# Kernel tuning notes

Hardware: AMD Instinct MI355X
Metric: run time of the kernel (lower is better)

Reference implementation:

```python
import jax, jax.numpy as jnp
import numpy as np

N_NODES = 100_000
D_FEAT = 512
N_EDGES = 3_200_000
L1, L2 = 32, 16
EPS = 1e-7


def setup_inputs() -> dict:
    key = jax.random.key(0)
    k = jax.random.split(key, 6)
    X = jax.random.normal(k[0], (N_NODES, D_FEAT), jnp.float32)
    # Xavier-uniform-ish init, as in get_weight_initial
    b1 = np.sqrt(6.0 / (D_FEAT + L1)).astype(np.float32)
    b2 = np.sqrt(6.0 / (L1 + L2)).astype(np.float32)
    W1 = jax.random.uniform(k[1], (D_FEAT, L1), jnp.float32, -b1, b1)
    W2 = jax.random.uniform(k[2], (L1, L2), jnp.float32, -b2, b2)
    lap_rows = jax.random.randint(k[3], (N_EDGES,), 0, N_NODES, jnp.int32)
    lap_cols = jax.random.randint(k[4], (N_EDGES,), 0, N_NODES, jnp.int32)
    # normalized-Laplacian values are small positives
    lap_vals = jax.random.uniform(k[5], (N_EDGES,), jnp.float32) * 0.1
    return {"X": X, "W1": W1, "W2": W2, "lap_rows": lap_rows,
            "lap_cols": lap_cols, "lap_vals": lap_vals}


def reference(X, W1, W2, lap_rows, lap_cols, lap_vals):
    n = X.shape[0]

    def spmm(H):  # Laplacian.mm(H): out[r] += val * H[c]
        return jax.ops.segment_sum(lap_vals[:, None] * H[lap_cols],
                                   lap_rows, num_segments=n)

    # layer 1: SpMM(X @ W1) -> relu
    H = jax.nn.relu(spmm(X @ W1))          # [N, 32]
    # layer 2: SpMM(H @ W2), final act is identity
    H = spmm(H @ W2)                        # [N, 16]
    # row-wise L2 normalization with eps clamp
    norm = jnp.linalg.norm(H, axis=1, keepdims=True)
    return H / jnp.maximum(norm, EPS)
```

## Files before the change

kernel.cpp:

```cpp
#include <hip/hip_runtime.h>
#include <math.h>

constexpr int NN = 100000;
constexpr int DF = 512;
constexpr int C1 = 32;
constexpr int C2 = 16;
constexpr long long NE = 3200000;
#define EPS_NORM 1e-7f

__global__ __launch_bounds__(256) void gemm1_k(const float* __restrict__ X,
                                               const float* __restrict__ W1,
                                               float* __restrict__ XW1) {
    int row = blockIdx.x * 256 + threadIdx.x;
    if (row >= NN) return;
    float acc[C1];
#pragma unroll
    for (int j = 0; j < C1; ++j) acc[j] = 0.f;
    const float4* xr = reinterpret_cast<const float4*>(X + (size_t)row * DF);
#pragma unroll 2
    for (int k4 = 0; k4 < DF / 4; ++k4) {
        float4 xv = xr[k4];
        const float* w = W1 + k4 * 4 * C1;
#pragma unroll
        for (int j = 0; j < C1; ++j) acc[j] = fmaf(xv.x, w[j], acc[j]);
#pragma unroll
        for (int j = 0; j < C1; ++j) acc[j] = fmaf(xv.y, w[C1 + j], acc[j]);
#pragma unroll
        for (int j = 0; j < C1; ++j) acc[j] = fmaf(xv.z, w[2 * C1 + j], acc[j]);
#pragma unroll
        for (int j = 0; j < C1; ++j) acc[j] = fmaf(xv.w, w[3 * C1 + j], acc[j]);
    }
    float4* o = reinterpret_cast<float4*>(XW1 + (size_t)row * C1);
#pragma unroll
    for (int q = 0; q < C1 / 4; ++q)
        o[q] = make_float4(acc[4 * q], acc[4 * q + 1], acc[4 * q + 2], acc[4 * q + 3]);
}

__global__ __launch_bounds__(256) void gemm2_k(const float* __restrict__ H1,
                                               const float* __restrict__ W2,
                                               float* __restrict__ HW2) {
    int row = blockIdx.x * 256 + threadIdx.x;
    if (row >= NN) return;
    float h[C1];
    const float4* hr = reinterpret_cast<const float4*>(H1 + (size_t)row * C1);
#pragma unroll
    for (int q = 0; q < C1 / 4; ++q) {
        float4 v = hr[q];
        h[4 * q + 0] = fmaxf(v.x, 0.f);
        h[4 * q + 1] = fmaxf(v.y, 0.f);
        h[4 * q + 2] = fmaxf(v.z, 0.f);
        h[4 * q + 3] = fmaxf(v.w, 0.f);
    }
    float acc[C2];
#pragma unroll
    for (int j = 0; j < C2; ++j) acc[j] = 0.f;
#pragma unroll
    for (int k = 0; k < C1; ++k) {
        const float* w = W2 + k * C2;
#pragma unroll
        for (int j = 0; j < C2; ++j) acc[j] = fmaf(h[k], w[j], acc[j]);
    }
    float4* o = reinterpret_cast<float4*>(HW2 + (size_t)row * C2);
#pragma unroll
    for (int q = 0; q < C2 / 4; ++q)
        o[q] = make_float4(acc[4 * q], acc[4 * q + 1], acc[4 * q + 2], acc[4 * q + 3]);
}

template <int F>
__global__ __launch_bounds__(256) void spmm_k(const int* __restrict__ rows,
                                              const int* __restrict__ cols,
                                              const float* __restrict__ vals,
                                              const float* __restrict__ Hin,
                                              float* __restrict__ Hout) {
    constexpr int SH = (F == 32) ? 5 : 4;
    constexpr int MSK = F - 1;
    long long total = NE << SH;
    long long stride = (long long)gridDim.x * 256;
    for (long long idx = (long long)blockIdx.x * 256 + threadIdx.x; idx < total;
         idx += stride) {
        int e = (int)(idx >> SH);
        int j = (int)(idx & MSK);
        int r = rows[e];
        int c = cols[e];
        float v = vals[e];
        float contrib = v * Hin[(size_t)c * F + j];
        unsafeAtomicAdd(&Hout[(size_t)r * F + j], contrib);
    }
}

__global__ __launch_bounds__(256) void norm_k(float* __restrict__ H) {
    int t = blockIdx.x * 256 + threadIdx.x;
    if (t >= NN * C2) return;
    float v = H[t];
    float s = v * v;
#pragma unroll
    for (int m = 1; m < C2; m <<= 1) s += __shfl_xor(s, m, C2);
    float norm = sqrtf(s);
    H[t] = v / fmaxf(norm, EPS_NORM);
}

extern "C" void kernel_launch(void* const* d_in, const int* in_sizes, int n_in,
                              void* d_out, int out_size, void* d_ws, size_t ws_size,
                              hipStream_t stream) {
    const float* X = (const float*)d_in[0];
    const float* W1 = (const float*)d_in[1];
    const float* W2 = (const float*)d_in[2];
    const int* lap_rows = (const int*)d_in[3];
    const int* lap_cols = (const int*)d_in[4];
    const float* vals = (const float*)d_in[5];
    float* out = (float*)d_out;

    float* XW1 = (float*)d_ws;
    float* H1 = XW1 + (size_t)NN * C1;
    float* HW2 = H1 + (size_t)NN * C1;

    hipMemsetAsync(H1, 0, (size_t)NN * C1 * sizeof(float), stream);
    hipMemsetAsync(out, 0, (size_t)NN * C2 * sizeof(float), stream);

    int rowBlocks = (NN + 255) / 256;
    gemm1_k<<<rowBlocks, 256, 0, stream>>>(X, W1, XW1);
    spmm_k<C1><<<16384, 256, 0, stream>>>(lap_rows, lap_cols, vals, XW1, H1);
    gemm2_k<<<rowBlocks, 256, 0, stream>>>(H1, W2, HW2);
    spmm_k<C2><<<8192, 256, 0, stream>>>(lap_rows, lap_cols, vals, HW2, out);
    norm_k<<<((NN * C2) + 255) / 256, 256, 0, stream>>>(out);
}
```

Baseline: 897.5 us.

## Build CSR bucket per call and replace atomic scatter SpMM with row-gather

Each call now builds a row-sorted edge bucket: a histogram, a three-kernel scan and an atomic scatter. Both SpMMs then become per-row gather kernels with one wavefront per row, with ReLU and the L2 normalization fused in, so the float atomics and memsets go away. The gemm kernels move to 64-thread blocks and batch eight float4 loads of X at a time. The cost is the per-call CSR construction, which needs extra workspace, plus an indirect bucket-to-edge lookup; if the workspace is too small the old path runs instead.

New measurement: 1.239 ms. 1.38x slower.

```diff
diff --git a/kernel.cpp b/kernel.cpp
--- a/kernel.cpp
+++ b/kernel.cpp
@@ -5,30 +5,38 @@
 constexpr int DF = 512;
 constexpr int C1 = 32;
 constexpr int C2 = 16;
-constexpr long long NE = 3200000;
+constexpr int NE = 3200000;
 #define EPS_NORM 1e-7f
 
-__global__ __launch_bounds__(256) void gemm1_k(const float* __restrict__ X,
-                                               const float* __restrict__ W1,
-                                               float* __restrict__ XW1) {
-    int row = blockIdx.x * 256 + threadIdx.x;
+constexpr int SCAN_B = 512;
+constexpr int SCAN_NBLK = (NN + SCAN_B - 1) / SCAN_B;
+
+__global__ __launch_bounds__(64) void gemm1_k(const float* __restrict__ X,
+                                              const float* __restrict__ W1,
+                                              float* __restrict__ XW1) {
+    int row = blockIdx.x * 64 + threadIdx.x;
     if (row >= NN) return;
     float acc[C1];
 #pragma unroll
     for (int j = 0; j < C1; ++j) acc[j] = 0.f;
     const float4* xr = reinterpret_cast<const float4*>(X + (size_t)row * DF);
-#pragma unroll 2
-    for (int k4 = 0; k4 < DF / 4; ++k4) {
-        float4 xv = xr[k4];
-        const float* w = W1 + k4 * 4 * C1;
-#pragma unroll
-        for (int j = 0; j < C1; ++j) acc[j] = fmaf(xv.x, w[j], acc[j]);
-#pragma unroll
-        for (int j = 0; j < C1; ++j) acc[j] = fmaf(xv.y, w[C1 + j], acc[j]);
-#pragma unroll
-        for (int j = 0; j < C1; ++j) acc[j] = fmaf(xv.z, w[2 * C1 + j], acc[j]);
-#pragma unroll
-        for (int j = 0; j < C1; ++j) acc[j] = fmaf(xv.w, w[3 * C1 + j], acc[j]);
+#pragma unroll 1
+    for (int k4 = 0; k4 < DF / 4; k4 += 8) {
+        float4 xv[8];
+#pragma unroll
+        for (int u = 0; u < 8; ++u) xv[u] = xr[k4 + u];
+#pragma unroll
+        for (int u = 0; u < 8; ++u) {
+            const float* w = W1 + (size_t)(k4 + u) * 4 * C1;
+#pragma unroll
+            for (int j = 0; j < C1; ++j) acc[j] = fmaf(xv[u].x, w[j], acc[j]);
+#pragma unroll
+            for (int j = 0; j < C1; ++j) acc[j] = fmaf(xv[u].y, w[C1 + j], acc[j]);
+#pragma unroll
+            for (int j = 0; j < C1; ++j) acc[j] = fmaf(xv[u].z, w[2 * C1 + j], acc[j]);
+#pragma unroll
+            for (int j = 0; j < C1; ++j) acc[j] = fmaf(xv[u].w, w[3 * C1 + j], acc[j]);
+        }
     }
     float4* o = reinterpret_cast<float4*>(XW1 + (size_t)row * C1);
 #pragma unroll
@@ -36,10 +44,10 @@
         o[q] = make_float4(acc[4 * q], acc[4 * q + 1], acc[4 * q + 2], acc[4 * q + 3]);
 }
 
-__global__ __launch_bounds__(256) void gemm2_k(const float* __restrict__ H1,
-                                               const float* __restrict__ W2,
-                                               float* __restrict__ HW2) {
-    int row = blockIdx.x * 256 + threadIdx.x;
+__global__ __launch_bounds__(64) void gemm2_k(const float* __restrict__ H1,
+                                              const float* __restrict__ W2,
+                                              float* __restrict__ HW2) {
+    int row = blockIdx.x * 64 + threadIdx.x;
     if (row >= NN) return;
     float h[C1];
     const float4* hr = reinterpret_cast<const float4*>(H1 + (size_t)row * C1);
@@ -64,6 +72,103 @@
 #pragma unroll
     for (int q = 0; q < C2 / 4; ++q)
         o[q] = make_float4(acc[4 * q], acc[4 * q + 1], acc[4 * q + 2], acc[4 * q + 3]);
+}
+
+__global__ __launch_bounds__(256) void hist_k(const int* __restrict__ rows,
+                                              int* __restrict__ cnt) {
+    int stride = gridDim.x * 256;
+    for (int e = blockIdx.x * 256 + threadIdx.x; e < NE; e += stride)
+        atomicAdd(&cnt[rows[e]], 1);
+}
+
+__global__ __launch_bounds__(SCAN_B) void scan1_k(const int* __restrict__ cnt,
+                                                  int* __restrict__ rowend,
+                                                  int* __restrict__ sums) {
+    __shared__ int sh[SCAN_B];
+    int t = threadIdx.x;
+    int g = blockIdx.x * SCAN_B + t;
+    sh[t] = (g < NN) ? cnt[g] : 0;
+    __syncthreads();
+#pragma unroll
+    for (int off = 1; off < SCAN_B; off <<= 1) {
+        int u = (t >= off) ? sh[t - off] : 0;
+        __syncthreads();
+        sh[t] += u;
+        __syncthreads();
+    }
+    if (g < NN) rowend[g] = sh[t];
+    if (t == SCAN_B - 1) sums[blockIdx.x] = sh[t];
+}
+
+__global__ __launch_bounds__(256) void scan2_k(int* __restrict__ sums) {
+    __shared__ int sh[256];
+    int t = threadIdx.x;
+    sh[t] = (t < SCAN_NBLK) ? sums[t] : 0;
+    __syncthreads();
+#pragma unroll
+    for (int off = 1; off < 256; off <<= 1) {
+        int u = (t >= off) ? sh[t - off] : 0;
+        __syncthreads();
+        sh[t] += u;
+        __syncthreads();
+    }
+    if (t < SCAN_NBLK) sums[t] = t ? sh[t - 1] : 0;
+}
+
+__global__ __launch_bounds__(SCAN_B) void scan3_k(const int* __restrict__ cnt,
+                                                  int* __restrict__ rowend,
+                                                  int* __restrict__ cursor,
+                                                  const int* __restrict__ sums) {
+    int g = blockIdx.x * SCAN_B + threadIdx.x;
+    if (g >= NN) return;
+    int e = rowend[g] + sums[blockIdx.x];
+    rowend[g] = e;
+    cursor[g] = e - cnt[g];
+}
+
+__global__ __launch_bounds__(256) void scatter_k(const int* __restrict__ rows,
+                                                 int* __restrict__ cursor,
+                                                 int* __restrict__ bucket) {
+    int stride = gridDim.x * 256;
+    for (int e = blockIdx.x * 256 + threadIdx.x; e < NE; e += stride) {
+        int pos = atomicAdd(&cursor[rows[e]], 1);
+        bucket[pos] = e;
+    }
+}
+
+template <int F, bool RELU, bool NORM>
+__global__ __launch_bounds__(256) void apply_k(const int* __restrict__ bucket,
+                                               const int* __restrict__ cols,
+                                               const float* __restrict__ vals,
+                                               const int* __restrict__ cnt,
+                                               const int* __restrict__ rowend,
+                                               const float* __restrict__ Hin,
+                                               float* __restrict__ Hout) {
+    constexpr int EPI = 64 / F;
+    int r = (blockIdx.x * 256 + threadIdx.x) >> 6;
+    if (r >= NN) return;
+    int lane = threadIdx.x & 63;
+    int j = lane & (F - 1);
+    int sub = lane >> ((F == 32) ? 5 : 4);
+    int end = rowend[r];
+    int start = end - cnt[r];
+    float acc = 0.f;
+    for (int i = start + sub; i < end; i += EPI) {
+        int e = bucket[i];
+        int c = cols[e];
+        float v = vals[e];
+        acc = fmaf(v, Hin[(size_t)c * F + j], acc);
+    }
+#pragma unroll
+    for (int m = F; m < 64; m <<= 1) acc += __shfl_xor(acc, m);
+    if (RELU) acc = fmaxf(acc, 0.f);
+    if (NORM) {
+        float s = acc * acc;
+#pragma unroll
+        for (int m = 1; m < F; m <<= 1) s += __shfl_xor(s, m);
+        acc = acc / fmaxf(sqrtf(s), EPS_NORM);
+    }
+    if (lane < F) Hout[(size_t)r * F + j] = acc;
 }
 
 template <int F>
@@ -74,17 +179,14 @@
                                               float* __restrict__ Hout) {
     constexpr int SH = (F == 32) ? 5 : 4;
     constexpr int MSK = F - 1;
-    long long total = NE << SH;
+    long long total = (long long)NE << SH;
     long long stride = (long long)gridDim.x * 256;
     for (long long idx = (long long)blockIdx.x * 256 + threadIdx.x; idx < total;
          idx += stride) {
         int e = (int)(idx >> SH);
         int j = (int)(idx & MSK);
-        int r = rows[e];
-        int c = cols[e];
-        float v = vals[e];
-        float contrib = v * Hin[(size_t)c * F + j];
-        unsafeAtomicAdd(&Hout[(size_t)r * F + j], contrib);
+        float contrib = vals[e] * Hin[(size_t)cols[e] * F + j];
+        unsafeAtomicAdd(&Hout[(size_t)rows[e] * F + j], contrib);
     }
 }
 
@@ -95,8 +197,7 @@
     float s = v * v;
 #pragma unroll
     for (int m = 1; m < C2; m <<= 1) s += __shfl_xor(s, m, C2);
-    float norm = sqrtf(s);
-    H[t] = v / fmaxf(norm, EPS_NORM);
+    H[t] = v / fmaxf(sqrtf(s), EPS_NORM);
 }
 
 extern "C" void kernel_launch(void* const* d_in, const int* in_sizes, int n_in,
@@ -113,14 +214,36 @@
     float* XW1 = (float*)d_ws;
     float* H1 = XW1 + (size_t)NN * C1;
     float* HW2 = H1 + (size_t)NN * C1;
-
-    hipMemsetAsync(H1, 0, (size_t)NN * C1 * sizeof(float), stream);
-    hipMemsetAsync(out, 0, (size_t)NN * C2 * sizeof(float), stream);
-
-    int rowBlocks = (NN + 255) / 256;
-    gemm1_k<<<rowBlocks, 256, 0, stream>>>(X, W1, XW1);
-    spmm_k<C1><<<16384, 256, 0, stream>>>(lap_rows, lap_cols, vals, XW1, H1);
-    gemm2_k<<<rowBlocks, 256, 0, stream>>>(H1, W2, HW2);
-    spmm_k<C2><<<8192, 256, 0, stream>>>(lap_rows, lap_cols, vals, HW2, out);
-    norm_k<<<((NN * C2) + 255) / 256, 256, 0, stream>>>(out);
-}
+    int* cnt = (int*)(HW2 + (size_t)NN * C2);
+    int* rowend = cnt + NN;
+    int* cursor = rowend + NN;
+    int* sums = cursor + NN;
+    int* bucket = sums + 256;
+    size_t need = (size_t)((char*)(bucket + NE) - (char*)d_ws);
+
+    int rowBlocks64 = (NN + 63) / 64;
+
+    if (ws_size >= need) {
+        hipMemsetAsync(cnt, 0, (size_t)NN * sizeof(int), stream);
+        hist_k<<<2048, 256, 0, stream>>>(lap_rows, cnt);
+        scan1_k<<<SCAN_NBLK, SCAN_B, 0, stream>>>(cnt, rowend, sums);
+        scan2_k<<<1, 256, 0, stream>>>(sums);
+        scan3_k<<<SCAN_NBLK, SCAN_B, 0, stream>>>(cnt, rowend, cursor, sums);
+        scatter_k<<<2048, 256, 0, stream>>>(lap_rows, cursor, bucket);
+
+        gemm1_k<<<rowBlocks64, 64, 0, stream>>>(X, W1, XW1);
+        apply_k<C1, true, false><<<(NN * 64 + 255) / 256, 256, 0, stream>>>(
+            bucket, lap_cols, vals, cnt, rowend, XW1, H1);
+        gemm2_k<<<rowBlocks64, 64, 0, stream>>>(H1, W2, HW2);
+        apply_k<C2, false, true><<<(NN * 64 + 255) / 256, 256, 0, stream>>>(
+            bucket, lap_cols, vals, cnt, rowend, HW2, out);
+    } else {
+        hipMemsetAsync(H1, 0, (size_t)NN * C1 * sizeof(float), stream);
+        hipMemsetAsync(out, 0, (size_t)NN * C2 * sizeof(float), stream);
+        gemm1_k<<<rowBlocks64, 64, 0, stream>>>(X, W1, XW1);
+        spmm_k<C1><<<16384, 256, 0, stream>>>(lap_rows, lap_cols, vals, XW1, H1);
+        gemm2_k<<<rowBlocks64, 64, 0, stream>>>(H1, W2, HW2);
+        spmm_k<C2><<<8192, 256, 0, stream>>>(lap_rows, lap_cols, vals, HW2, out);
+        norm_k<<<((NN * C2) + 255) / 256, 256, 0, stream>>>(out);
+    }
+}
```

## Bucket edges by destination row block and accumulate SpMM in shared memory

Applied to the files above, without the earlier changes.

Edges are counting-sorted into 256-row buckets (histogram, two scans, scatter), packing column and local row into one word. Each SpMM then runs one block per bucket, accumulating in LDS with shared atomics instead of global atomics, and fuses ReLU+GEMM2 into the first SpMM and the L2 normalization into the second. GEMM1 also stages X through a padded shared tile for coalesced loads. This removes the global atomic traffic and the memsets, at the cost of a per-call sort pass over all edges and larger workspace, with a fallback to the old path if the workspace is too small.

Result: slower. 1.582 ms (+76.3%).

```diff
diff --git a/kernel.cpp b/kernel.cpp
--- a/kernel.cpp
+++ b/kernel.cpp
@@ -5,41 +5,222 @@
 constexpr int DF = 512;
 constexpr int C1 = 32;
 constexpr int C2 = 16;
-constexpr long long NE = 3200000;
+constexpr int NE = 3200000;
 #define EPS_NORM 1e-7f
+
+constexpr int BKT = 256;
+constexpr int NBKT = (NN + BKT - 1) / BKT;
+constexpr int NCH = 256;
+constexpr int CHUNK = NE / NCH;
 
 __global__ __launch_bounds__(256) void gemm1_k(const float* __restrict__ X,
                                                const float* __restrict__ W1,
                                                float* __restrict__ XW1) {
-    int row = blockIdx.x * 256 + threadIdx.x;
-    if (row >= NN) return;
+    __shared__ float tile[256 * 33];
+    int t = threadIdx.x;
+    int rowbase = blockIdx.x * 256;
     float acc[C1];
 #pragma unroll
     for (int j = 0; j < C1; ++j) acc[j] = 0.f;
-    const float4* xr = reinterpret_cast<const float4*>(X + (size_t)row * DF);
-#pragma unroll 2
-    for (int k4 = 0; k4 < DF / 4; ++k4) {
-        float4 xv = xr[k4];
-        const float* w = W1 + k4 * 4 * C1;
-#pragma unroll
-        for (int j = 0; j < C1; ++j) acc[j] = fmaf(xv.x, w[j], acc[j]);
-#pragma unroll
-        for (int j = 0; j < C1; ++j) acc[j] = fmaf(xv.y, w[C1 + j], acc[j]);
-#pragma unroll
-        for (int j = 0; j < C1; ++j) acc[j] = fmaf(xv.z, w[2 * C1 + j], acc[j]);
-#pragma unroll
-        for (int j = 0; j < C1; ++j) acc[j] = fmaf(xv.w, w[3 * C1 + j], acc[j]);
-    }
-    float4* o = reinterpret_cast<float4*>(XW1 + (size_t)row * C1);
-#pragma unroll
-    for (int q = 0; q < C1 / 4; ++q)
-        o[q] = make_float4(acc[4 * q], acc[4 * q + 1], acc[4 * q + 2], acc[4 * q + 3]);
-}
-
-__global__ __launch_bounds__(256) void gemm2_k(const float* __restrict__ H1,
-                                               const float* __restrict__ W2,
-                                               float* __restrict__ HW2) {
-    int row = blockIdx.x * 256 + threadIdx.x;
+    for (int c = 0; c < DF / 32; ++c) {
+        __syncthreads();
+#pragma unroll
+        for (int i = 0; i < 8; ++i) {
+            int li = i * 256 + t;
+            int row = li >> 3;
+            int o4 = (li & 7) * 4;
+            int grow = rowbase + row;
+            float4 v = make_float4(0.f, 0.f, 0.f, 0.f);
+            if (grow < NN)
+                v = *reinterpret_cast<const float4*>(X + (size_t)grow * DF + c * 32 + o4);
+            tile[row * 33 + o4 + 0] = v.x;
+            tile[row * 33 + o4 + 1] = v.y;
+            tile[row * 33 + o4 + 2] = v.z;
+            tile[row * 33 + o4 + 3] = v.w;
+        }
+        __syncthreads();
+        const float* wb = W1 + c * 32 * C1;
+#pragma unroll
+        for (int k = 0; k < 32; ++k) {
+            float xv = tile[t * 33 + k];
+            const float* w = wb + k * C1;
+#pragma unroll
+            for (int j = 0; j < C1; ++j) acc[j] = fmaf(xv, w[j], acc[j]);
+        }
+    }
+    int grow = rowbase + t;
+    if (grow < NN) {
+        float4* o = reinterpret_cast<float4*>(XW1 + (size_t)grow * C1);
+#pragma unroll
+        for (int q = 0; q < C1 / 4; ++q)
+            o[q] = make_float4(acc[4 * q], acc[4 * q + 1], acc[4 * q + 2], acc[4 * q + 3]);
+    }
+}
+
+__global__ __launch_bounds__(256) void bh_k(const int* __restrict__ rows,
+                                            int* __restrict__ blkcnt) {
+    __shared__ int lh[NBKT];
+    int t = threadIdx.x, bi = blockIdx.x;
+    for (int i = t; i < NBKT; i += 256) lh[i] = 0;
+    __syncthreads();
+    int base = bi * CHUNK;
+    for (int i = t; i < CHUNK; i += 256)
+        atomicAdd(&lh[rows[base + i] >> 8], 1);
+    __syncthreads();
+    for (int i = t; i < NBKT; i += 256) blkcnt[i * NCH + bi] = lh[i];
+}
+
+__global__ __launch_bounds__(NCH) void bscan_k(int* __restrict__ blkcnt,
+                                               int* __restrict__ bkttot) {
+    __shared__ int sh[NCH];
+    int t = threadIdx.x, b = blockIdx.x;
+    int v = blkcnt[b * NCH + t];
+    sh[t] = v;
+    __syncthreads();
+#pragma unroll
+    for (int off = 1; off < NCH; off <<= 1) {
+        int u = (t >= off) ? sh[t - off] : 0;
+        __syncthreads();
+        sh[t] += u;
+        __syncthreads();
+    }
+    blkcnt[b * NCH + t] = sh[t] - v;
+    if (t == NCH - 1) bkttot[b] = sh[t];
+}
+
+__global__ __launch_bounds__(512) void bscan2_k(const int* __restrict__ bkttot,
+                                                int* __restrict__ bktstart) {
+    __shared__ int sh[512];
+    int t = threadIdx.x;
+    sh[t] = (t < NBKT) ? bkttot[t] : 0;
+    __syncthreads();
+#pragma unroll
+    for (int off = 1; off < 512; off <<= 1) {
+        int u = (t >= off) ? sh[t - off] : 0;
+        __syncthreads();
+        sh[t] += u;
+        __syncthreads();
+    }
+    if (t < NBKT) bktstart[t] = (t == 0) ? 0 : sh[t - 1];
+    if (t == 0) bktstart[NBKT] = NE;
+}
+
+__global__ __launch_bounds__(256) void bfill_k(const int* __restrict__ rows,
+                                               const int* __restrict__ cols,
+                                               const float* __restrict__ vals,
+                                               const int* __restrict__ blkcnt,
+                                               const int* __restrict__ bktstart,
+                                               unsigned int* __restrict__ bpack,
+                                               float* __restrict__ bval) {
+    __shared__ int cur[NBKT];
+    int t = threadIdx.x, bi = blockIdx.x;
+    for (int i = t; i < NBKT; i += 256) cur[i] = 0;
+    __syncthreads();
+    int base = bi * CHUNK;
+    for (int i = t; i < CHUNK; i += 256) {
+        int e = base + i;
+        int r = rows[e];
+        int bkt = r >> 8;
+        int rank = atomicAdd(&cur[bkt], 1);
+        int dst = bktstart[bkt] + blkcnt[bkt * NCH + bi] + rank;
+        bpack[dst] = ((unsigned)cols[e] << 8) | (unsigned)(r & 255);
+        bval[dst] = vals[e];
+    }
+}
+
+__global__ __launch_bounds__(512) void apply1_k(const unsigned int* __restrict__ bpack,
+                                                const float* __restrict__ bval,
+                                                const int* __restrict__ bktstart,
+                                                const float* __restrict__ XW1,
+                                                const float* __restrict__ W2,
+                                                float* __restrict__ HW2) {
+    __shared__ float acc[256 * 33];
+    int t = threadIdx.x, b = blockIdx.x;
+    for (int i = t; i < 256 * 33; i += 512) acc[i] = 0.f;
+    __syncthreads();
+    int base = bktstart[b], end = bktstart[b + 1];
+    int sub = t >> 5, j = t & 31;
+    int i = base + sub;
+    for (; i + 7 * 16 < end; i += 8 * 16) {
+        unsigned p[8]; float v[8];
+#pragma unroll
+        for (int u = 0; u < 8; ++u) { p[u] = bpack[i + u * 16]; v[u] = bval[i + u * 16]; }
+        float x[8];
+#pragma unroll
+        for (int u = 0; u < 8; ++u) x[u] = XW1[(size_t)(p[u] >> 8) * C1 + j];
+#pragma unroll
+        for (int u = 0; u < 8; ++u) atomicAdd(&acc[(p[u] & 255u) * 33 + j], v[u] * x[u]);
+    }
+    for (; i < end; i += 16) {
+        unsigned p = bpack[i]; float v = bval[i];
+        float x = XW1[(size_t)(p >> 8) * C1 + j];
+        atomicAdd(&acc[(p & 255u) * 33 + j], v * x);
+    }
+    __syncthreads();
+    int grow = b * 256 + t;
+    if (t < 256 && grow < NN) {
+        float h[C1];
+#pragma unroll
+        for (int k = 0; k < C1; ++k) h[k] = fmaxf(acc[t * 33 + k], 0.f);
+        float o[C2];
+#pragma unroll
+        for (int q = 0; q < C2; ++q) o[q] = 0.f;
+#pragma unroll
+        for (int k = 0; k < C1; ++k) {
+            const float* w = W2 + k * C2;
+#pragma unroll
+            for (int q = 0; q < C2; ++q) o[q] = fmaf(h[k], w[q], o[q]);
+        }
+        float4* op = reinterpret_cast<float4*>(HW2 + (size_t)grow * C2);
+#pragma unroll
+        for (int q = 0; q < C2 / 4; ++q)
+            op[q] = make_float4(o[4 * q], o[4 * q + 1], o[4 * q + 2], o[4 * q + 3]);
+    }
+}
+
+__global__ __launch_bounds__(512) void apply2_k(const unsigned int* __restrict__ bpack,
+                                                const float* __restrict__ bval,
+                                                const int* __restrict__ bktstart,
+                                                const float* __restrict__ HW2,
+                                                float* __restrict__ out) {
+    __shared__ float acc[256 * 17];
+    int t = threadIdx.x, b = blockIdx.x;
+    for (int i = t; i < 256 * 17; i += 512) acc[i] = 0.f;
+    __syncthreads();
+    int base = bktstart[b], end = bktstart[b + 1];
+    int sub = t >> 4, j = t & 15;
+    int i = base + sub;
+    for (; i + 7 * 32 < end; i += 8 * 32) {
+        unsigned p[8]; float v[8];
+#pragma unroll
+        for (int u = 0; u < 8; ++u) { p[u] = bpack[i + u * 32]; v[u] = bval[i + u * 32]; }
+        float x[8];
+#pragma unroll
+        for (int u = 0; u < 8; ++u) x[u] = HW2[(size_t)(p[u] >> 8) * C2 + j];
+#pragma unroll
+        for (int u = 0; u < 8; ++u) atomicAdd(&acc[(p[u] & 255u) * 17 + j], v[u] * x[u]);
+    }
+    for (; i < end; i += 32) {
+        unsigned p = bpack[i]; float v = bval[i];
+        float x = HW2[(size_t)(p >> 8) * C2 + j];
+        atomicAdd(&acc[(p & 255u) * 17 + j], v * x);
+    }
+    __syncthreads();
+    for (int r = (t >> 4); r < 256; r += 32) {
+        int grow = b * 256 + r;
+        if (grow >= NN) break;
+        float val = acc[r * 17 + j];
+        float s = val * val;
+#pragma unroll
+        for (int m = 1; m < 16; m <<= 1) s += __shfl_xor(s, m);
+        out[(size_t)grow * C2 + j] = val / fmaxf(sqrtf(s), EPS_NORM);
+    }
+}
+
+__global__ __launch_bounds__(64) void gemm2_k(const float* __restrict__ H1,
+                                              const float* __restrict__ W2,
+                                              float* __restrict__ HW2) {
+    int row = blockIdx.x * 64 + threadIdx.x;
     if (row >= NN) return;
     float h[C1];
     const float4* hr = reinterpret_cast<const float4*>(H1 + (size_t)row * C1);
@@ -74,17 +255,14 @@
                                               float* __restrict__ Hout) {
     constexpr int SH = (F == 32) ? 5 : 4;
     constexpr int MSK = F - 1;
-    long long total = NE << SH;
+    long long total = (long long)NE << SH;
     long long stride = (long long)gridDim.x * 256;
     for (long long idx = (long long)blockIdx.x * 256 + threadIdx.x; idx < total;
          idx += stride) {
         int e = (int)(idx >> SH);
         int j = (int)(idx & MSK);
-        int r = rows[e];
-        int c = cols[e];
-        float v = vals[e];
-        float contrib = v * Hin[(size_t)c * F + j];
-        unsafeAtomicAdd(&Hout[(size_t)r * F + j], contrib);
+        float contrib = vals[e] * Hin[(size_t)cols[e] * F + j];
+        unsafeAtomicAdd(&Hout[(size_t)rows[e] * F + j], contrib);
     }
 }
 
@@ -95,8 +273,7 @@
     float s = v * v;
 #pragma unroll
     for (int m = 1; m < C2; m <<= 1) s += __shfl_xor(s, m, C2);
-    float norm = sqrtf(s);
-    H[t] = v / fmaxf(norm, EPS_NORM);
+    H[t] = v / fmaxf(sqrtf(s), EPS_NORM);
 }
 
 extern "C" void kernel_launch(void* const* d_in, const int* in_sizes, int n_in,
@@ -111,16 +288,31 @@
     float* out = (float*)d_out;
 
     float* XW1 = (float*)d_ws;
-    float* H1 = XW1 + (size_t)NN * C1;
-    float* HW2 = H1 + (size_t)NN * C1;
-
-    hipMemsetAsync(H1, 0, (size_t)NN * C1 * sizeof(float), stream);
-    hipMemsetAsync(out, 0, (size_t)NN * C2 * sizeof(float), stream);
-
-    int rowBlocks = (NN + 255) / 256;
-    gemm1_k<<<rowBlocks, 256, 0, stream>>>(X, W1, XW1);
-    spmm_k<C1><<<16384, 256, 0, stream>>>(lap_rows, lap_cols, vals, XW1, H1);
-    gemm2_k<<<rowBlocks, 256, 0, stream>>>(H1, W2, HW2);
-    spmm_k<C2><<<8192, 256, 0, stream>>>(lap_rows, lap_cols, vals, HW2, out);
-    norm_k<<<((NN * C2) + 255) / 256, 256, 0, stream>>>(out);
-}
+    float* HW2 = XW1 + (size_t)NN * C1;
+    unsigned int* bpack = (unsigned int*)(HW2 + (size_t)NN * C2);
+    float* bval = (float*)(bpack + NE);
+    int* blkcnt = (int*)(bval + NE);
+    int* bkttot = blkcnt + NBKT * NCH;
+    int* bktstart = bkttot + NBKT;
+    size_t need = (size_t)((char*)(bktstart + NBKT + 1) - (char*)d_ws);
+
+    if (ws_size >= need) {
+        bh_k<<<NCH, 256, 0, stream>>>(lap_rows, blkcnt);
+        bscan_k<<<NBKT, NCH, 0, stream>>>(blkcnt, bkttot);
+        bscan2_k<<<1, 512, 0, stream>>>(bkttot, bktstart);
+        bfill_k<<<NCH, 256, 0, stream>>>(lap_rows, lap_cols, vals, blkcnt,
+                                         bktstart, bpack, bval);
+        gemm1_k<<<(NN + 255) / 256, 256, 0, stream>>>(X, W1, XW1);
+        apply1_k<<<NBKT, 512, 0, stream>>>(bpack, bval, bktstart, XW1, W2, HW2);
+        apply2_k<<<NBKT, 512, 0, stream>>>(bpack, bval, bktstart, HW2, out);
+    } else {
+        float* H1 = (float*)bpack;
+        hipMemsetAsync(H1, 0, (size_t)NN * C1 * sizeof(float), stream);
+        hipMemsetAsync(out, 0, (size_t)NN * C2 * sizeof(float), stream);
+        gemm1_k<<<(NN + 255) / 256, 256, 0, stream>>>(X, W1, XW1);
+        spmm_k<C1><<<16384, 256, 0, stream>>>(lap_rows, lap_cols, vals, XW1, H1);
+        gemm2_k<<<(NN + 63) / 64, 64, 0, stream>>>(H1, W2, HW2);
+        spmm_k<C2><<<8192, 256, 0, stream>>>(lap_rows, lap_cols, vals, HW2, out);
+        norm_k<<<((NN * C2) + 255) / 256, 256, 0, stream>>>(out);
+    }
+}
```
